# Optimization experiments

Measured on AMD Instinct MI355X. Metric: run time of the kernel, lower is better.

The kernel has to match this reference:

```python
import jax, jax.numpy as jnp
import numpy as np

B, OUT_LEN, IN_LEN, H = 8, 1024, 4096, 256


def setup_inputs() -> dict:
    key = jax.random.key(0)
    k1, k2, k3 = jax.random.split(key, 3)
    output = jax.random.normal(k1, (B, OUT_LEN, H), dtype=jnp.float32)
    encoder_outputs = jax.random.normal(k2, (B, IN_LEN, H), dtype=jnp.float32)
    # valid lengths in [1, IN_LEN] so every softmax row has >=1 unmasked entry
    lengths = jax.random.randint(k3, (B,), 1, IN_LEN + 1).astype(jnp.int32)
    return {"output": output, "encoder_outputs": encoder_outputs, "lengths": lengths}


def reference(output, encoder_outputs, lengths):
    # scores: [B, out_len, in_len], unscaled dot-product (as in the original)
    scores = jnp.einsum('boh,bih->boi', output, encoder_outputs)
    # mask[b, j] = j < lengths[b]; masked positions get -inf (additive mask)
    valid = jnp.arange(encoder_outputs.shape[1])[None, :] < lengths[:, None]  # [B, in_len]
    scores = jnp.where(valid[:, None, :], scores, -jnp.inf)
    attn = jax.nn.softmax(scores, axis=-1)  # [B, out_len, in_len]
    context = jnp.einsum('boi,bih->boh', attn, encoder_outputs)  # [B, out_len, H]
    return (context, attn)
```

## Files before the change

### kernel.cpp

```cpp
#include <hip/hip_runtime.h>
#include <hip/hip_bf16.h>
#include <math.h>

#define B_    8
#define OLEN  1024
#define ILEN  4096
#define HDIM  256
#define LDA   40

typedef __attribute__((ext_vector_type(8))) short bf16x8;
typedef __attribute__((ext_vector_type(4))) float f32x4;

__device__ inline unsigned pk_bf16(float x, float y) {
  union { __hip_bfloat162 h; unsigned u; } c;
  c.h = __float22bfloat162_rn(make_float2(x, y));
  return c.u;
}
__device__ inline short f2bf(float x) {
  union { __hip_bfloat16 h; short s; } c;
  c.h = __float2bfloat16(x);
  return c.s;
}

struct HiLo { uint4 hi, lo; };
__device__ inline HiLo split8(const float* __restrict__ p) {
  float4 v0 = *(const float4*)p;
  float4 v1 = *(const float4*)(p + 4);
  float f[8] = {v0.x, v0.y, v0.z, v0.w, v1.x, v1.y, v1.z, v1.w};
  unsigned hu[8]; float lo[8];
#pragma unroll
  for (int i = 0; i < 8; ++i) {
    unsigned u = __float_as_uint(f[i]);
    hu[i] = u & 0xffff0000u;
    lo[i] = f[i] - __uint_as_float(hu[i]);
  }
  HiLo r;
  r.hi = make_uint4((hu[0] >> 16) | hu[1], (hu[2] >> 16) | hu[3],
                    (hu[4] >> 16) | hu[5], (hu[6] >> 16) | hu[7]);
  r.lo = make_uint4(pk_bf16(lo[0], lo[1]), pk_bf16(lo[2], lo[3]),
                    pk_bf16(lo[4], lo[5]), pk_bf16(lo[6], lo[7]));
  return r;
}

__device__ inline void gl_lds16(const void* g, void* l) {
  __builtin_amdgcn_global_load_lds(
      (const __attribute__((address_space(1))) unsigned*)g,
      (__attribute__((address_space(3))) unsigned*)(l), 16, 0, 0);
}

__global__ __launch_bounds__(256) void k_prep_q(const float* __restrict__ Q,
                                                short* __restrict__ Qhi,
                                                short* __restrict__ Qlo) {
  const size_t idx = ((size_t)blockIdx.x * 256 + threadIdx.x) * 8;
  HiLo r = split8(&Q[idx]);
  *(uint4*)&Qhi[idx] = r.hi;
  *(uint4*)&Qlo[idx] = r.lo;
}

__global__ __launch_bounds__(256) void k_prep_e(const float* __restrict__ E,
                                                short* __restrict__ Ehi,
                                                short* __restrict__ Elo,
                                                short* __restrict__ ET) {
  const int it = blockIdx.x, ht = blockIdx.y, b = blockIdx.z;
  __shared__ short L[32][36];
  const int t = threadIdx.x;
  {
    const int i = t >> 3, h0 = (t & 7) * 4;
    const size_t gidx = ((size_t)(b * ILEN + it * 32 + i)) * HDIM + ht * 32 + h0;
    float4 v = *(const float4*)&E[gidx];
    float f[4] = {v.x, v.y, v.z, v.w};
    unsigned hs[4]; float lo[4];
#pragma unroll
    for (int j = 0; j < 4; ++j) {
      unsigned u = __float_as_uint(f[j]);
      hs[j] = u & 0xffff0000u;
      lo[j] = f[j] - __uint_as_float(hs[j]);
    }
    *(uint2*)&Ehi[gidx] = make_uint2((hs[0] >> 16) | hs[1], (hs[2] >> 16) | hs[3]);
    *(uint2*)&Elo[gidx] = make_uint2(pk_bf16(lo[0], lo[1]), pk_bf16(lo[2], lo[3]));
    L[h0 + 0][i] = f2bf(f[0]);
    L[h0 + 1][i] = f2bf(f[1]);
    L[h0 + 2][i] = f2bf(f[2]);
    L[h0 + 3][i] = f2bf(f[3]);
  }
  __syncthreads();
  {
    const int h = t >> 3, i0 = (t & 7) * 4;
    *(uint2*)&ET[((size_t)(b * HDIM + ht * 32 + h)) * ILEN + it * 32 + i0] =
        *(const uint2*)&L[h][i0];
  }
}

__global__ __launch_bounds__(256) void k_scores_pre(
    const short* __restrict__ Qhi, const short* __restrict__ Qlo,
    const short* __restrict__ Ehi, const short* __restrict__ Elo,
    float* __restrict__ S) {
  const int it = blockIdx.x, ot = blockIdx.y, b = blockIdx.z;
  const size_t qoff = ((size_t)b * OLEN + ot * 128) * HDIM;
  const size_t eoff = ((size_t)b * ILEN + it * 128) * HDIM;

  __shared__ __align__(16) short Ah[128 * 32], Al[128 * 32];
  __shared__ __align__(16) short Bh[128 * 32], Bl[128 * 32];

  const int t = threadIdx.x;
  const int w = t >> 6, l = t & 63;
  const int la = l & 15, quad = l >> 4;
  const int mw = (w & 1) * 64, nw = (w >> 1) * 64;

  int sgoff[2], sloff[2];
#pragma unroll
  for (int j = 0; j < 2; ++j) {
    const int row = (w * 2 + j) * 16 + (l >> 2);
    const int c = (l & 3) ^ ((row >> 1) & 3);
    sgoff[j] = row * HDIM + c * 8;
    sloff[j] = ((w * 2 + j) * 64 + l) * 8;
  }

  f32x4 acc[4][4] = {};

  for (int kc = 0; kc < HDIM; kc += 32) {
#pragma unroll
    for (int j = 0; j < 2; ++j) {
      const size_t ga = qoff + sgoff[j] + kc;
      const size_t gb = eoff + sgoff[j] + kc;
      gl_lds16(&Qhi[ga], &Ah[sloff[j]]);
      gl_lds16(&Qlo[ga], &Al[sloff[j]]);
      gl_lds16(&Ehi[gb], &Bh[sloff[j]]);
      gl_lds16(&Elo[gb], &Bl[sloff[j]]);
    }
    __syncthreads();
    bf16x8 ah[4], al[4];
#pragma unroll
    for (int mi = 0; mi < 4; ++mi) {
      const int row = mw + mi * 16 + la;
      const int off = row * 32 + (quad ^ ((row >> 1) & 3)) * 8;
      ah[mi] = *(const bf16x8*)&Ah[off];
      al[mi] = *(const bf16x8*)&Al[off];
    }
#pragma unroll
    for (int ni = 0; ni < 4; ++ni) {
      const int row = nw + ni * 16 + la;
      const int off = row * 32 + (quad ^ ((row >> 1) & 3)) * 8;
      bf16x8 bh = *(const bf16x8*)&Bh[off];
      bf16x8 bl = *(const bf16x8*)&Bl[off];
#pragma unroll
      for (int mi = 0; mi < 4; ++mi) {
        acc[mi][ni] = __builtin_amdgcn_mfma_f32_16x16x32_bf16(ah[mi], bh, acc[mi][ni], 0, 0, 0);
        acc[mi][ni] = __builtin_amdgcn_mfma_f32_16x16x32_bf16(ah[mi], bl, acc[mi][ni], 0, 0, 0);
        acc[mi][ni] = __builtin_amdgcn_mfma_f32_16x16x32_bf16(al[mi], bh, acc[mi][ni], 0, 0, 0);
      }
    }
    __syncthreads();
  }

  float* Sb = S + ((size_t)b * OLEN + ot * 128) * (size_t)ILEN + it * 128;
#pragma unroll
  for (int mi = 0; mi < 4; ++mi)
#pragma unroll
    for (int ni = 0; ni < 4; ++ni)
#pragma unroll
      for (int r = 0; r < 4; ++r)
        Sb[(size_t)(mw + mi * 16 + quad * 4 + r) * ILEN + nw + ni * 16 + la] =
            acc[mi][ni][r];
}

__global__ __launch_bounds__(256) void k_scores_split(const float* __restrict__ Q,
                                                      const float* __restrict__ E,
                                                      float* __restrict__ S) {
  const int b = blockIdx.z, ot = blockIdx.y, it = blockIdx.x;
  const float* Qb = Q + ((size_t)b * OLEN + ot * 64) * HDIM;
  const float* Eb = E + ((size_t)b * ILEN + it * 64) * HDIM;

  __shared__ __align__(16) short Ah[64 * LDA], Al[64 * LDA];
  __shared__ __align__(16) short Bh[64 * LDA], Bl[64 * LDA];

  const int t = threadIdx.x;
  const int w = t >> 6, l = t & 63;
  const int la = l & 15, quad = l >> 4;
  const int sr = t >> 2, sc = (t & 3) * 8;

  f32x4 acc[4] = {};

#pragma unroll
  for (int kc = 0; kc < HDIM; kc += 32) {
    HiLo qa = split8(&Qb[(size_t)sr * HDIM + kc + sc]);
    HiLo eb = split8(&Eb[(size_t)sr * HDIM + kc + sc]);
    *(uint4*)&Ah[sr * LDA + sc] = qa.hi;
    *(uint4*)&Al[sr * LDA + sc] = qa.lo;
    *(uint4*)&Bh[sr * LDA + sc] = eb.hi;
    *(uint4*)&Bl[sr * LDA + sc] = eb.lo;
    __syncthreads();
    bf16x8 ah = *(const bf16x8*)&Ah[(w * 16 + la) * LDA + quad * 8];
    bf16x8 al = *(const bf16x8*)&Al[(w * 16 + la) * LDA + quad * 8];
#pragma unroll
    for (int n = 0; n < 4; ++n) {
      bf16x8 bh = *(const bf16x8*)&Bh[(n * 16 + la) * LDA + quad * 8];
      bf16x8 bl = *(const bf16x8*)&Bl[(n * 16 + la) * LDA + quad * 8];
      acc[n] = __builtin_amdgcn_mfma_f32_16x16x32_bf16(ah, bh, acc[n], 0, 0, 0);
      acc[n] = __builtin_amdgcn_mfma_f32_16x16x32_bf16(ah, bl, acc[n], 0, 0, 0);
      acc[n] = __builtin_amdgcn_mfma_f32_16x16x32_bf16(al, bh, acc[n], 0, 0, 0);
    }
    __syncthreads();
  }

  float* Sb = S + ((size_t)b * OLEN + ot * 64) * (size_t)ILEN + it * 64;
#pragma unroll
  for (int n = 0; n < 4; ++n)
#pragma unroll
    for (int r = 0; r < 4; ++r)
      Sb[(size_t)(w * 16 + quad * 4 + r) * ILEN + n * 16 + la] = acc[n][r];
}

__global__ __launch_bounds__(256) void k_softmax(float* __restrict__ A,
                                                 const int* __restrict__ len) {
  const int row = blockIdx.x;
  const int b   = row >> 10;
  const int L   = len[b];
  float* p = A + (size_t)row * ILEN;
  const int t = threadIdx.x;

  float v[16];
#pragma unroll
  for (int k = 0; k < 4; ++k) {
    float4 x = *(const float4*)&p[4 * t + 1024 * k];
    v[4 * k + 0] = x.x; v[4 * k + 1] = x.y;
    v[4 * k + 2] = x.z; v[4 * k + 3] = x.w;
  }

  float m = -INFINITY;
#pragma unroll
  for (int k = 0; k < 4; ++k)
#pragma unroll
    for (int j = 0; j < 4; ++j) {
      const int i = 4 * t + 1024 * k + j;
      if (i < L) m = fmaxf(m, v[4 * k + j]);
    }
  for (int o = 32; o > 0; o >>= 1) m = fmaxf(m, __shfl_xor(m, o, 64));
  __shared__ float sm[4], ss[4];
  const int w = t >> 6;
  if ((t & 63) == 0) sm[w] = m;
  __syncthreads();
  m = fmaxf(fmaxf(sm[0], sm[1]), fmaxf(sm[2], sm[3]));

  float s = 0.f;
#pragma unroll
  for (int k = 0; k < 4; ++k)
#pragma unroll
    for (int j = 0; j < 4; ++j) {
      const int i = 4 * t + 1024 * k + j;
      float pv = (i < L) ? __expf(v[4 * k + j] - m) : 0.f;
      v[4 * k + j] = pv;
      s += pv;
    }
  for (int o = 32; o > 0; o >>= 1) s += __shfl_xor(s, o, 64);
  if ((t & 63) == 0) ss[w] = s;
  __syncthreads();
  s = ss[0] + ss[1] + ss[2] + ss[3];
  const float inv = 1.f / s;

#pragma unroll
  for (int k = 0; k < 4; ++k) {
    float4 x = make_float4(v[4 * k + 0] * inv, v[4 * k + 1] * inv,
                           v[4 * k + 2] * inv, v[4 * k + 3] * inv);
    *(float4*)&p[4 * t + 1024 * k] = x;
  }
}

__global__ __launch_bounds__(256) void k_context(const float* __restrict__ P,
                                                 const short* __restrict__ ET,
                                                 float* __restrict__ C) {
  const int ot = blockIdx.x, ht = blockIdx.y, b = blockIdx.z;
  const float* Pb = P + ((size_t)b * OLEN + ot * 64) * (size_t)ILEN;
  const short* Tb = ET + ((size_t)b * HDIM + ht * 64) * (size_t)ILEN;

  __shared__ __align__(16) short As[64 * LDA], Bs[64 * LDA];

  const int t = threadIdx.x;
  const int w = t >> 6, l = t & 63;
  const int la = l & 15, quad = l >> 4;
  const int sr = t >> 2, sc = (t & 3) * 8;

  f32x4 acc[4] = {};

  for (int ic = 0; ic < ILEN; ic += 32) {
    {
      float4 p0 = *(const float4*)&Pb[(size_t)sr * ILEN + ic + sc];
      float4 p1 = *(const float4*)&Pb[(size_t)sr * ILEN + ic + sc + 4];
      uint4 aw = make_uint4(pk_bf16(p0.x, p0.y), pk_bf16(p0.z, p0.w),
                            pk_bf16(p1.x, p1.y), pk_bf16(p1.z, p1.w));
      *(uint4*)&As[sr * LDA + sc] = aw;
      uint4 bw = *(const uint4*)&Tb[(size_t)sr * ILEN + ic + sc];
      *(uint4*)&Bs[sr * LDA + sc] = bw;
    }
    __syncthreads();
    bf16x8 a = *(const bf16x8*)&As[(w * 16 + la) * LDA + quad * 8];
#pragma unroll
    for (int n = 0; n < 4; ++n) {
      bf16x8 bb = *(const bf16x8*)&Bs[(n * 16 + la) * LDA + quad * 8];
      acc[n] = __builtin_amdgcn_mfma_f32_16x16x32_bf16(a, bb, acc[n], 0, 0, 0);
    }
    __syncthreads();
  }

  float* Cb = C + ((size_t)b * OLEN + ot * 64) * HDIM + ht * 64;
#pragma unroll
  for (int n = 0; n < 4; ++n)
#pragma unroll
    for (int r = 0; r < 4; ++r)
      Cb[(size_t)(w * 16 + quad * 4 + r) * HDIM + n * 16 + la] = acc[n][r];
}

extern "C" void kernel_launch(void* const* d_in, const int* in_sizes, int n_in,
                              void* d_out, int out_size, void* d_ws, size_t ws_size,
                              hipStream_t stream) {
  (void)in_sizes; (void)n_in; (void)out_size;
  const float* outp = (const float*)d_in[0];
  const float* enc  = (const float*)d_in[1];
  const int*   len  = (const int*)d_in[2];

  float* ctx  = (float*)d_out;
  float* attn = ctx + (size_t)B_ * OLEN * HDIM;

  short* ws = (short*)d_ws;
  const size_t M = 1024 * 1024;
  short* ET = ws;

  if (ws_size >= 56ull * 1024 * 1024) {
    short* Qhi = ws + 8 * M;
    short* Qlo = ws + 10 * M;
    short* Ehi = ws + 12 * M;
    short* Elo = ws + 20 * M;
    k_prep_q<<<(B_ * OLEN * HDIM) / (256 * 8), 256, 0, stream>>>(outp, Qhi, Qlo);
    dim3 gp(ILEN / 32, HDIM / 32, B_);
    k_prep_e<<<gp, 256, 0, stream>>>(enc, Ehi, Elo, ET);
    dim3 g1(ILEN / 128, OLEN / 128, B_);
    k_scores_pre<<<g1, 256, 0, stream>>>(Qhi, Qlo, Ehi, Elo, attn);
  } else {
    dim3 gp(ILEN / 32, HDIM / 32, B_);
    k_prep_e<<<gp, 256, 0, stream>>>(enc, ET, ET, ET);
    k_scores_split<<<dim3(ILEN / 64, OLEN / 64, B_), 256, 0, stream>>>(outp, enc, attn);
  }
  k_softmax<<<B_ * OLEN, 256, 0, stream>>>(attn, len);
  dim3 g3(OLEN / 64, HDIM / 64, B_);
  k_context<<<g3, 256, 0, stream>>>(attn, ET, ctx);
}
```

Before: 333.3 us.

## Emit bf16 copy of attention in softmax and feed a swizzled-LDS context GEMM

The softmax now also writes a bf16 copy of the probabilities to workspace. A new context kernel reads that copy through direct global-to-LDS loads, using an XOR-swizzled 64-wide K tile and a 2x2 MFMA tile per wave, in place of re-reading and converting the fp32 attention matrix. This halves the context GEMM's read traffic on the attention matrix at the cost of an extra 64MB write in softmax. The path is gated on a larger workspace threshold (90MB), so with a smaller workspace it falls back to the fp32 path, and the fallback gets a dedicated transpose kernel.

After: 359.5 us. +7.9%, slower.

```diff
diff --git a/kernel.cpp b/kernel.cpp
--- a/kernel.cpp
+++ b/kernel.cpp
@@ -164,6 +164,155 @@
             acc[mi][ni][r];
 }
 
+__global__ __launch_bounds__(256) void k_softmax_bf(float* __restrict__ A,
+                                                    short* __restrict__ Pbf,
+                                                    const int* __restrict__ len) {
+  const int row = blockIdx.x;
+  const int b   = row >> 10;
+  const int L   = len[b];
+  float* p = A + (size_t)row * ILEN;
+  short* q = Pbf + (size_t)row * ILEN;
+  const int t = threadIdx.x;
+
+  float v[16];
+#pragma unroll
+  for (int k = 0; k < 4; ++k) {
+    float4 x = *(const float4*)&p[4 * t + 1024 * k];
+    v[4 * k + 0] = x.x; v[4 * k + 1] = x.y;
+    v[4 * k + 2] = x.z; v[4 * k + 3] = x.w;
+  }
+
+  float m = -INFINITY;
+#pragma unroll
+  for (int k = 0; k < 4; ++k)
+#pragma unroll
+    for (int j = 0; j < 4; ++j) {
+      const int i = 4 * t + 1024 * k + j;
+      if (i < L) m = fmaxf(m, v[4 * k + j]);
+    }
+  for (int o = 32; o > 0; o >>= 1) m = fmaxf(m, __shfl_xor(m, o, 64));
+  __shared__ float sm[4], ss[4];
+  const int w = t >> 6;
+  if ((t & 63) == 0) sm[w] = m;
+  __syncthreads();
+  m = fmaxf(fmaxf(sm[0], sm[1]), fmaxf(sm[2], sm[3]));
+
+  float s = 0.f;
+#pragma unroll
+  for (int k = 0; k < 4; ++k)
+#pragma unroll
+    for (int j = 0; j < 4; ++j) {
+      const int i = 4 * t + 1024 * k + j;
+      float pv = (i < L) ? __expf(v[4 * k + j] - m) : 0.f;
+      v[4 * k + j] = pv;
+      s += pv;
+    }
+  for (int o = 32; o > 0; o >>= 1) s += __shfl_xor(s, o, 64);
+  if ((t & 63) == 0) ss[w] = s;
+  __syncthreads();
+  s = ss[0] + ss[1] + ss[2] + ss[3];
+  const float inv = 1.f / s;
+
+#pragma unroll
+  for (int k = 0; k < 4; ++k) {
+    float4 x = make_float4(v[4 * k + 0] * inv, v[4 * k + 1] * inv,
+                           v[4 * k + 2] * inv, v[4 * k + 3] * inv);
+    *(float4*)&p[4 * t + 1024 * k] = x;
+    *(uint2*)&q[4 * t + 1024 * k] = make_uint2(pk_bf16(x.x, x.y), pk_bf16(x.z, x.w));
+  }
+}
+
+__global__ __launch_bounds__(256) void k_context_pre(const short* __restrict__ Pbf,
+                                                     const short* __restrict__ ET,
+                                                     float* __restrict__ C) {
+  const int ot = blockIdx.x, ht = blockIdx.y, b = blockIdx.z;
+  const short* Pb = Pbf + ((size_t)b * OLEN + ot * 64) * (size_t)ILEN;
+  const short* Tb = ET  + ((size_t)b * HDIM + ht * 64) * (size_t)ILEN;
+
+  __shared__ __align__(16) short As[64 * 64], Bs[64 * 64];
+
+  const int t = threadIdx.x;
+  const int w = t >> 6, l = t & 63;
+  const int la = l & 15, quad = l >> 4;
+  const int mw = (w & 1) * 32, nw = (w >> 1) * 32;
+
+  int sg[2], sl[2];
+#pragma unroll
+  for (int j = 0; j < 2; ++j) {
+    const int slot = j * 256 + t;
+    const int row = slot >> 3, pc = slot & 7;
+    const int c = pc ^ (row & 7);
+    sg[j] = row * ILEN + c * 8;
+    sl[j] = slot * 8;
+  }
+
+  f32x4 acc[2][2] = {};
+
+  for (int ic = 0; ic < ILEN; ic += 64) {
+#pragma unroll
+    for (int j = 0; j < 2; ++j) {
+      gl_lds16(&Pb[sg[j] + ic], &As[sl[j]]);
+      gl_lds16(&Tb[sg[j] + ic], &Bs[sl[j]]);
+    }
+    __syncthreads();
+    bf16x8 af[2][2], bfr[2][2];
+#pragma unroll
+    for (int mi = 0; mi < 2; ++mi)
+#pragma unroll
+      for (int ki = 0; ki < 2; ++ki) {
+        const int row = mw + mi * 16 + la;
+        af[mi][ki] = *(const bf16x8*)&As[row * 64 + (((ki * 4 + quad) ^ (row & 7)) * 8)];
+      }
+#pragma unroll
+    for (int ni = 0; ni < 2; ++ni)
+#pragma unroll
+      for (int ki = 0; ki < 2; ++ki) {
+        const int row = nw + ni * 16 + la;
+        bfr[ni][ki] = *(const bf16x8*)&Bs[row * 64 + (((ki * 4 + quad) ^ (row & 7)) * 8)];
+      }
+#pragma unroll
+    for (int mi = 0; mi < 2; ++mi)
+#pragma unroll
+      for (int ni = 0; ni < 2; ++ni)
+#pragma unroll
+        for (int ki = 0; ki < 2; ++ki)
+          acc[mi][ni] = __builtin_amdgcn_mfma_f32_16x16x32_bf16(af[mi][ki], bfr[ni][ki],
+                                                                acc[mi][ni], 0, 0, 0);
+    __syncthreads();
+  }
+
+  float* Cb = C + ((size_t)b * OLEN + ot * 64) * HDIM + ht * 64;
+#pragma unroll
+  for (int mi = 0; mi < 2; ++mi)
+#pragma unroll
+    for (int ni = 0; ni < 2; ++ni)
+#pragma unroll
+      for (int r = 0; r < 4; ++r)
+        Cb[(size_t)(mw + mi * 16 + quad * 4 + r) * HDIM + nw + ni * 16 + la] =
+            acc[mi][ni][r];
+}
+
+__global__ __launch_bounds__(256) void k_etrans(const float* __restrict__ E,
+                                                short* __restrict__ ET) {
+  const int it = blockIdx.x, ht = blockIdx.y, b = blockIdx.z;
+  __shared__ short L[32][36];
+  const int t = threadIdx.x;
+  {
+    const int i = t >> 3, h0 = (t & 7) * 4;
+    float4 v = *(const float4*)&E[((size_t)(b * ILEN + it * 32 + i)) * HDIM + ht * 32 + h0];
+    L[h0 + 0][i] = f2bf(v.x);
+    L[h0 + 1][i] = f2bf(v.y);
+    L[h0 + 2][i] = f2bf(v.z);
+    L[h0 + 3][i] = f2bf(v.w);
+  }
+  __syncthreads();
+  {
+    const int h = t >> 3, i0 = (t & 7) * 4;
+    *(uint2*)&ET[((size_t)(b * HDIM + ht * 32 + h)) * ILEN + it * 32 + i0] =
+        *(const uint2*)&L[h][i0];
+  }
+}
+
 __global__ __launch_bounds__(256) void k_scores_split(const float* __restrict__ Q,
                                                       const float* __restrict__ E,
                                                       float* __restrict__ S) {
@@ -211,64 +360,9 @@
       Sb[(size_t)(w * 16 + quad * 4 + r) * ILEN + n * 16 + la] = acc[n][r];
 }
 
-__global__ __launch_bounds__(256) void k_softmax(float* __restrict__ A,
-                                                 const int* __restrict__ len) {
-  const int row = blockIdx.x;
-  const int b   = row >> 10;
-  const int L   = len[b];
-  float* p = A + (size_t)row * ILEN;
-  const int t = threadIdx.x;
-
-  float v[16];
-#pragma unroll
-  for (int k = 0; k < 4; ++k) {
-    float4 x = *(const float4*)&p[4 * t + 1024 * k];
-    v[4 * k + 0] = x.x; v[4 * k + 1] = x.y;
-    v[4 * k + 2] = x.z; v[4 * k + 3] = x.w;
-  }
-
-  float m = -INFINITY;
-#pragma unroll
-  for (int k = 0; k < 4; ++k)
-#pragma unroll
-    for (int j = 0; j < 4; ++j) {
-      const int i = 4 * t + 1024 * k + j;
-      if (i < L) m = fmaxf(m, v[4 * k + j]);
-    }
-  for (int o = 32; o > 0; o >>= 1) m = fmaxf(m, __shfl_xor(m, o, 64));
-  __shared__ float sm[4], ss[4];
-  const int w = t >> 6;
-  if ((t & 63) == 0) sm[w] = m;
-  __syncthreads();
-  m = fmaxf(fmaxf(sm[0], sm[1]), fmaxf(sm[2], sm[3]));
-
-  float s = 0.f;
-#pragma unroll
-  for (int k = 0; k < 4; ++k)
-#pragma unroll
-    for (int j = 0; j < 4; ++j) {
-      const int i = 4 * t + 1024 * k + j;
-      float pv = (i < L) ? __expf(v[4 * k + j] - m) : 0.f;
-      v[4 * k + j] = pv;
-      s += pv;
-    }
-  for (int o = 32; o > 0; o >>= 1) s += __shfl_xor(s, o, 64);
-  if ((t & 63) == 0) ss[w] = s;
-  __syncthreads();
-  s = ss[0] + ss[1] + ss[2] + ss[3];
-  const float inv = 1.f / s;
-
-#pragma unroll
-  for (int k = 0; k < 4; ++k) {
-    float4 x = make_float4(v[4 * k + 0] * inv, v[4 * k + 1] * inv,
-                           v[4 * k + 2] * inv, v[4 * k + 3] * inv);
-    *(float4*)&p[4 * t + 1024 * k] = x;
-  }
-}
-
-__global__ __launch_bounds__(256) void k_context(const float* __restrict__ P,
-                                                 const short* __restrict__ ET,
-                                                 float* __restrict__ C) {
+__global__ __launch_bounds__(256) void k_context_f32(const float* __restrict__ P,
+                                                     const short* __restrict__ ET,
+                                                     float* __restrict__ C) {
   const int ot = blockIdx.x, ht = blockIdx.y, b = blockIdx.z;
   const float* Pb = P + ((size_t)b * OLEN + ot * 64) * (size_t)ILEN;
   const short* Tb = ET + ((size_t)b * HDIM + ht * 64) * (size_t)ILEN;
@@ -310,6 +404,58 @@
       Cb[(size_t)(w * 16 + quad * 4 + r) * HDIM + n * 16 + la] = acc[n][r];
 }
 
+__global__ __launch_bounds__(256) void k_softmax(float* __restrict__ A,
+                                                 const int* __restrict__ len) {
+  const int row = blockIdx.x;
+  const int b   = row >> 10;
+  const int L   = len[b];
+  float* p = A + (size_t)row * ILEN;
+  const int t = threadIdx.x;
+
+  float v[16];
+#pragma unroll
+  for (int k = 0; k < 4; ++k) {
+    float4 x = *(const float4*)&p[4 * t + 1024 * k];
+    v[4 * k + 0] = x.x; v[4 * k + 1] = x.y;
+    v[4 * k + 2] = x.z; v[4 * k + 3] = x.w;
+  }
+  float m = -INFINITY;
+#pragma unroll
+  for (int k = 0; k < 4; ++k)
+#pragma unroll
+    for (int j = 0; j < 4; ++j) {
+      const int i = 4 * t + 1024 * k + j;
+      if (i < L) m = fmaxf(m, v[4 * k + j]);
+    }
+  for (int o = 32; o > 0; o >>= 1) m = fmaxf(m, __shfl_xor(m, o, 64));
+  __shared__ float sm[4], ss[4];
+  const int w = t >> 6;
+  if ((t & 63) == 0) sm[w] = m;
+  __syncthreads();
+  m = fmaxf(fmaxf(sm[0], sm[1]), fmaxf(sm[2], sm[3]));
+  float s = 0.f;
+#pragma unroll
+  for (int k = 0; k < 4; ++k)
+#pragma unroll
+    for (int j = 0; j < 4; ++j) {
+      const int i = 4 * t + 1024 * k + j;
+      float pv = (i < L) ? __expf(v[4 * k + j] - m) : 0.f;
+      v[4 * k + j] = pv;
+      s += pv;
+    }
+  for (int o = 32; o > 0; o >>= 1) s += __shfl_xor(s, o, 64);
+  if ((t & 63) == 0) ss[w] = s;
+  __syncthreads();
+  s = ss[0] + ss[1] + ss[2] + ss[3];
+  const float inv = 1.f / s;
+#pragma unroll
+  for (int k = 0; k < 4; ++k) {
+    float4 x = make_float4(v[4 * k + 0] * inv, v[4 * k + 1] * inv,
+                           v[4 * k + 2] * inv, v[4 * k + 3] * inv);
+    *(float4*)&p[4 * t + 1024 * k] = x;
+  }
+}
+
 extern "C" void kernel_launch(void* const* d_in, const int* in_sizes, int n_in,
                               void* d_out, int out_size, void* d_ws, size_t ws_size,
                               hipStream_t stream) {
@@ -325,22 +471,26 @@
   const size_t M = 1024 * 1024;
   short* ET = ws;
 
-  if (ws_size >= 56ull * 1024 * 1024) {
+  if (ws_size >= 90ull * 1024 * 1024) {
     short* Qhi = ws + 8 * M;
     short* Qlo = ws + 10 * M;
     short* Ehi = ws + 12 * M;
     short* Elo = ws + 20 * M;
+    short* Pbf = ws + 28 * M;
     k_prep_q<<<(B_ * OLEN * HDIM) / (256 * 8), 256, 0, stream>>>(outp, Qhi, Qlo);
     dim3 gp(ILEN / 32, HDIM / 32, B_);
     k_prep_e<<<gp, 256, 0, stream>>>(enc, Ehi, Elo, ET);
     dim3 g1(ILEN / 128, OLEN / 128, B_);
     k_scores_pre<<<g1, 256, 0, stream>>>(Qhi, Qlo, Ehi, Elo, attn);
+    k_softmax_bf<<<B_ * OLEN, 256, 0, stream>>>(attn, Pbf, len);
+    dim3 g3(OLEN / 64, HDIM / 64, B_);
+    k_context_pre<<<g3, 256, 0, stream>>>(Pbf, ET, ctx);
   } else {
-    dim3 gp(ILEN / 32, HDIM / 32, B_);
-    k_prep_e<<<gp, 256, 0, stream>>>(enc, ET, ET, ET);
+    dim3 gt(ILEN / 32, HDIM / 32, B_);
+    k_etrans<<<gt, 256, 0, stream>>>(enc, ET);
     k_scores_split<<<dim3(ILEN / 64, OLEN / 64, B_), 256, 0, stream>>>(outp, enc, attn);
-  }
-  k_softmax<<<B_ * OLEN, 256, 0, stream>>>(attn, len);
-  dim3 g3(OLEN / 64, HDIM / 64, B_);
-  k_context<<<g3, 256, 0, stream>>>(attn, ET, ctx);
-}
+    k_softmax<<<B_ * OLEN, 256, 0, stream>>>(attn, len);
+    dim3 g3(OLEN / 64, HDIM / 64, B_);
+    k_context_f32<<<g3, 256, 0, stream>>>(attn, ET, ctx);
+  }
+}
```

## Retile context GEMM with full-H tiles, swizzled LDS, split-K and reduce

Applied to the files above, without the earlier changes.

Replaces the context kernel on the large-workspace path. The new kernel covers all 256 hidden columns per block, so each attention tile is read from global memory once. It stages tiles in XOR-swizzled LDS, using direct global-to-LDS loads for the transposed encoder, and splits the input dimension in two, writing partial sums that a small reduce kernel adds. This removes the fourfold re-read of the fp32 attention matrix across hidden tiles, at the cost of a partial-sum buffer round trip and one extra launch. The fallback path gets a dedicated transpose kernel instead of reusing prep_e.

After: 318.5 us. 1.05x faster.

```diff
diff --git a/kernel.cpp b/kernel.cpp
--- a/kernel.cpp
+++ b/kernel.cpp
@@ -164,6 +164,169 @@
             acc[mi][ni][r];
 }
 
+__global__ __launch_bounds__(256) void k_softmax(float* __restrict__ A,
+                                                 const int* __restrict__ len) {
+  const int row = blockIdx.x;
+  const int b   = row >> 10;
+  const int L   = len[b];
+  float* p = A + (size_t)row * ILEN;
+  const int t = threadIdx.x;
+
+  float v[16];
+#pragma unroll
+  for (int k = 0; k < 4; ++k) {
+    float4 x = *(const float4*)&p[4 * t + 1024 * k];
+    v[4 * k + 0] = x.x; v[4 * k + 1] = x.y;
+    v[4 * k + 2] = x.z; v[4 * k + 3] = x.w;
+  }
+  float m = -INFINITY;
+#pragma unroll
+  for (int k = 0; k < 4; ++k)
+#pragma unroll
+    for (int j = 0; j < 4; ++j) {
+      const int i = 4 * t + 1024 * k + j;
+      if (i < L) m = fmaxf(m, v[4 * k + j]);
+    }
+  for (int o = 32; o > 0; o >>= 1) m = fmaxf(m, __shfl_xor(m, o, 64));
+  __shared__ float sm[4], ss[4];
+  const int w = t >> 6;
+  if ((t & 63) == 0) sm[w] = m;
+  __syncthreads();
+  m = fmaxf(fmaxf(sm[0], sm[1]), fmaxf(sm[2], sm[3]));
+  float s = 0.f;
+#pragma unroll
+  for (int k = 0; k < 4; ++k)
+#pragma unroll
+    for (int j = 0; j < 4; ++j) {
+      const int i = 4 * t + 1024 * k + j;
+      float pv = (i < L) ? __expf(v[4 * k + j] - m) : 0.f;
+      v[4 * k + j] = pv;
+      s += pv;
+    }
+  for (int o = 32; o > 0; o >>= 1) s += __shfl_xor(s, o, 64);
+  if ((t & 63) == 0) ss[w] = s;
+  __syncthreads();
+  s = ss[0] + ss[1] + ss[2] + ss[3];
+  const float inv = 1.f / s;
+#pragma unroll
+  for (int k = 0; k < 4; ++k) {
+    float4 x = make_float4(v[4 * k + 0] * inv, v[4 * k + 1] * inv,
+                           v[4 * k + 2] * inv, v[4 * k + 3] * inv);
+    *(float4*)&p[4 * t + 1024 * k] = x;
+  }
+}
+
+__global__ __launch_bounds__(256) void k_context_v3(const float* __restrict__ P,
+                                                    const short* __restrict__ ET,
+                                                    float* __restrict__ Cpart) {
+  const int ot = blockIdx.x, ks = blockIdx.y, b = blockIdx.z;
+  const float* Pb = P + ((size_t)b * OLEN + ot * 64) * (size_t)ILEN + ks * 2048;
+  const short* Tb = ET + (size_t)b * HDIM * ILEN + ks * 2048;
+
+  __shared__ __align__(16) short As[64 * 64];
+  __shared__ __align__(16) short Bs[256 * 64];
+
+  const int t = threadIdx.x;
+  const int w = t >> 6, l = t & 63;
+  const int la = l & 15, quad = l >> 4;
+  const int mw = (w & 1) * 32, nw = (w >> 1) * 128;
+
+  const int tr = t >> 2, tc = t & 3;
+  const int ac0 = tc * 2;
+  int bslot[8];
+#pragma unroll
+  for (int j = 0; j < 8; ++j) bslot[j] = w * 512 + j * 64 + l;
+
+  f32x4 acc[2][8] = {};
+
+  for (int ic = 0; ic < 2048; ic += 64) {
+#pragma unroll
+    for (int j = 0; j < 8; ++j) {
+      const int s = bslot[j];
+      const int row = s >> 3, pc = s & 7;
+      const int c = pc ^ (row & 7);
+      gl_lds16(&Tb[(size_t)row * ILEN + ic + c * 8], &Bs[s * 8]);
+    }
+    {
+      const float* src = &Pb[(size_t)tr * ILEN + ic + tc * 16];
+      float4 f0 = *(const float4*)src;
+      float4 f1 = *(const float4*)(src + 4);
+      float4 f2 = *(const float4*)(src + 8);
+      float4 f3 = *(const float4*)(src + 12);
+      uint4 w0 = make_uint4(pk_bf16(f0.x, f0.y), pk_bf16(f0.z, f0.w),
+                            pk_bf16(f1.x, f1.y), pk_bf16(f1.z, f1.w));
+      uint4 w1 = make_uint4(pk_bf16(f2.x, f2.y), pk_bf16(f2.z, f2.w),
+                            pk_bf16(f3.x, f3.y), pk_bf16(f3.z, f3.w));
+      *(uint4*)&As[tr * 64 + ((ac0) ^ (tr & 7)) * 8] = w0;
+      *(uint4*)&As[tr * 64 + ((ac0 + 1) ^ (tr & 7)) * 8] = w1;
+    }
+    __syncthreads();
+#pragma unroll
+    for (int ki = 0; ki < 2; ++ki) {
+      bf16x8 af[2];
+#pragma unroll
+      for (int mi = 0; mi < 2; ++mi) {
+        const int row = mw + mi * 16 + la;
+        af[mi] = *(const bf16x8*)&As[row * 64 + ((ki * 4 + quad) ^ (row & 7)) * 8];
+      }
+#pragma unroll
+      for (int ni = 0; ni < 8; ++ni) {
+        const int row = nw + ni * 16 + la;
+        bf16x8 bfr = *(const bf16x8*)&Bs[row * 64 + ((ki * 4 + quad) ^ (row & 7)) * 8];
+#pragma unroll
+        for (int mi = 0; mi < 2; ++mi)
+          acc[mi][ni] = __builtin_amdgcn_mfma_f32_16x16x32_bf16(af[mi], bfr,
+                                                               acc[mi][ni], 0, 0, 0);
+      }
+    }
+    __syncthreads();
+  }
+
+  float* Cb = Cpart + (size_t)ks * (B_ * OLEN * HDIM) +
+              ((size_t)b * OLEN + ot * 64) * HDIM;
+#pragma unroll
+  for (int mi = 0; mi < 2; ++mi)
+#pragma unroll
+    for (int ni = 0; ni < 8; ++ni)
+#pragma unroll
+      for (int r = 0; r < 4; ++r)
+        Cb[(size_t)(mw + mi * 16 + quad * 4 + r) * HDIM + nw + ni * 16 + la] =
+            acc[mi][ni][r];
+}
+
+__global__ __launch_bounds__(256) void k_reduce(const float* __restrict__ Cp,
+                                                float* __restrict__ ctx) {
+  const size_t idx = ((size_t)blockIdx.x * 256 + threadIdx.x) * 8;
+  const size_t n = (size_t)B_ * OLEN * HDIM;
+  float4 a0 = *(const float4*)&Cp[idx];
+  float4 a1 = *(const float4*)&Cp[idx + 4];
+  float4 b0 = *(const float4*)&Cp[n + idx];
+  float4 b1 = *(const float4*)&Cp[n + idx + 4];
+  *(float4*)&ctx[idx] = make_float4(a0.x + b0.x, a0.y + b0.y, a0.z + b0.z, a0.w + b0.w);
+  *(float4*)&ctx[idx + 4] = make_float4(a1.x + b1.x, a1.y + b1.y, a1.z + b1.z, a1.w + b1.w);
+}
+
+__global__ __launch_bounds__(256) void k_etrans(const float* __restrict__ E,
+                                                short* __restrict__ ET) {
+  const int it = blockIdx.x, ht = blockIdx.y, b = blockIdx.z;
+  __shared__ short L[32][36];
+  const int t = threadIdx.x;
+  {
+    const int i = t >> 3, h0 = (t & 7) * 4;
+    float4 v = *(const float4*)&E[((size_t)(b * ILEN + it * 32 + i)) * HDIM + ht * 32 + h0];
+    L[h0 + 0][i] = f2bf(v.x);
+    L[h0 + 1][i] = f2bf(v.y);
+    L[h0 + 2][i] = f2bf(v.z);
+    L[h0 + 3][i] = f2bf(v.w);
+  }
+  __syncthreads();
+  {
+    const int h = t >> 3, i0 = (t & 7) * 4;
+    *(uint2*)&ET[((size_t)(b * HDIM + ht * 32 + h)) * ILEN + it * 32 + i0] =
+        *(const uint2*)&L[h][i0];
+  }
+}
+
 __global__ __launch_bounds__(256) void k_scores_split(const float* __restrict__ Q,
                                                       const float* __restrict__ E,
                                                       float* __restrict__ S) {
@@ -211,64 +374,9 @@
       Sb[(size_t)(w * 16 + quad * 4 + r) * ILEN + n * 16 + la] = acc[n][r];
 }
 
-__global__ __launch_bounds__(256) void k_softmax(float* __restrict__ A,
-                                                 const int* __restrict__ len) {
-  const int row = blockIdx.x;
-  const int b   = row >> 10;
-  const int L   = len[b];
-  float* p = A + (size_t)row * ILEN;
-  const int t = threadIdx.x;
-
-  float v[16];
-#pragma unroll
-  for (int k = 0; k < 4; ++k) {
-    float4 x = *(const float4*)&p[4 * t + 1024 * k];
-    v[4 * k + 0] = x.x; v[4 * k + 1] = x.y;
-    v[4 * k + 2] = x.z; v[4 * k + 3] = x.w;
-  }
-
-  float m = -INFINITY;
-#pragma unroll
-  for (int k = 0; k < 4; ++k)
-#pragma unroll
-    for (int j = 0; j < 4; ++j) {
-      const int i = 4 * t + 1024 * k + j;
-      if (i < L) m = fmaxf(m, v[4 * k + j]);
-    }
-  for (int o = 32; o > 0; o >>= 1) m = fmaxf(m, __shfl_xor(m, o, 64));
-  __shared__ float sm[4], ss[4];
-  const int w = t >> 6;
-  if ((t & 63) == 0) sm[w] = m;
-  __syncthreads();
-  m = fmaxf(fmaxf(sm[0], sm[1]), fmaxf(sm[2], sm[3]));
-
-  float s = 0.f;
-#pragma unroll
-  for (int k = 0; k < 4; ++k)
-#pragma unroll
-    for (int j = 0; j < 4; ++j) {
-      const int i = 4 * t + 1024 * k + j;
-      float pv = (i < L) ? __expf(v[4 * k + j] - m) : 0.f;
-      v[4 * k + j] = pv;
-      s += pv;
-    }
-  for (int o = 32; o > 0; o >>= 1) s += __shfl_xor(s, o, 64);
-  if ((t & 63) == 0) ss[w] = s;
-  __syncthreads();
-  s = ss[0] + ss[1] + ss[2] + ss[3];
-  const float inv = 1.f / s;
-
-#pragma unroll
-  for (int k = 0; k < 4; ++k) {
-    float4 x = make_float4(v[4 * k + 0] * inv, v[4 * k + 1] * inv,
-                           v[4 * k + 2] * inv, v[4 * k + 3] * inv);
-    *(float4*)&p[4 * t + 1024 * k] = x;
-  }
-}
-
-__global__ __launch_bounds__(256) void k_context(const float* __restrict__ P,
-                                                 const short* __restrict__ ET,
-                                                 float* __restrict__ C) {
+__global__ __launch_bounds__(256) void k_context_f32(const float* __restrict__ P,
+                                                     const short* __restrict__ ET,
+                                                     float* __restrict__ C) {
   const int ot = blockIdx.x, ht = blockIdx.y, b = blockIdx.z;
   const float* Pb = P + ((size_t)b * OLEN + ot * 64) * (size_t)ILEN;
   const short* Tb = ET + ((size_t)b * HDIM + ht * 64) * (size_t)ILEN;
@@ -330,17 +438,22 @@
     short* Qlo = ws + 10 * M;
     short* Ehi = ws + 12 * M;
     short* Elo = ws + 20 * M;
+    float* Cpart = (float*)(ws + 8 * M);
     k_prep_q<<<(B_ * OLEN * HDIM) / (256 * 8), 256, 0, stream>>>(outp, Qhi, Qlo);
     dim3 gp(ILEN / 32, HDIM / 32, B_);
     k_prep_e<<<gp, 256, 0, stream>>>(enc, Ehi, Elo, ET);
     dim3 g1(ILEN / 128, OLEN / 128, B_);
     k_scores_pre<<<g1, 256, 0, stream>>>(Qhi, Qlo, Ehi, Elo, attn);
+    k_softmax<<<B_ * OLEN, 256, 0, stream>>>(attn, len);
+    dim3 g3(OLEN / 64, 2, B_);
+    k_context_v3<<<g3, 256, 0, stream>>>(attn, ET, Cpart);
+    k_reduce<<<(B_ * OLEN * HDIM) / (256 * 8), 256, 0, stream>>>(Cpart, ctx);
   } else {
-    dim3 gp(ILEN / 32, HDIM / 32, B_);
-    k_prep_e<<<gp, 256, 0, stream>>>(enc, ET, ET, ET);
+    dim3 gt(ILEN / 32, HDIM / 32, B_);
+    k_etrans<<<gt, 256, 0, stream>>>(enc, ET);
     k_scores_split<<<dim3(ILEN / 64, OLEN / 64, B_), 256, 0, stream>>>(outp, enc, attn);
-  }
-  k_softmax<<<B_ * OLEN, 256, 0, stream>>>(attn, len);
-  dim3 g3(OLEN / 64, HDIM / 64, B_);
-  k_context<<<g3, 256, 0, stream>>>(attn, ET, ctx);
-}
+    k_softmax<<<B_ * OLEN, 256, 0, stream>>>(attn, len);
+    dim3 g3(OLEN / 64, HDIM / 64, B_);
+    k_context_f32<<<g3, 256, 0, stream>>>(attn, ET, ctx);
+  }
+}
```
